# Optimization experiments

Hardware: AMD Instinct MI355X
Metric: run time of the kernel (lower is better)

## Reference

```python
import jax, jax.numpy as jnp
import numpy as np

N = 40000
E = 200000
D = 32
NUM_BANDS = 3
ORDER = 4
EPS = 1e-8
LN_EPS = 1e-5


def setup_inputs() -> dict:
    key = jax.random.key(0)
    ks = jax.random.split(key, 20)
    h = jax.random.normal(ks[0], (N, D), dtype=jnp.float32)
    Q = jax.random.normal(ks[1], (E, D, D), dtype=jnp.float32) / jnp.sqrt(jnp.float32(D))
    edge_index = jax.random.randint(ks[2], (2, E), 0, N, dtype=jnp.int32)
    coeffs = jnp.ones((NUM_BANDS, ORDER + 1), dtype=jnp.float32) / (ORDER + 1)
    s = 1.0 / np.sqrt(D)
    proj_W = jax.random.uniform(ks[3], (NUM_BANDS, D, D), minval=-s, maxval=s, dtype=jnp.float32)
    proj_b = jax.random.uniform(ks[4], (NUM_BANDS, D), minval=-s, maxval=s, dtype=jnp.float32)
    proj_g = jnp.ones((NUM_BANDS, D), dtype=jnp.float32)
    proj_beta = jnp.zeros((NUM_BANDS, D), dtype=jnp.float32)
    s3 = 1.0 / np.sqrt(NUM_BANDS * D)
    fus_W1 = jax.random.uniform(ks[5], (NUM_BANDS * D, D), minval=-s3, maxval=s3, dtype=jnp.float32)
    fus_b1 = jax.random.uniform(ks[6], (D,), minval=-s3, maxval=s3, dtype=jnp.float32)
    fus_g = jnp.ones((D,), dtype=jnp.float32)
    fus_beta = jnp.zeros((D,), dtype=jnp.float32)
    fus_W2 = jax.random.uniform(ks[7], (D, D), minval=-s, maxval=s, dtype=jnp.float32)
    fus_b2 = jax.random.uniform(ks[8], (D,), minval=-s, maxval=s, dtype=jnp.float32)
    return {"h": h, "Q": Q, "edge_index": edge_index, "coeffs": coeffs,
            "proj_W": proj_W, "proj_b": proj_b, "proj_g": proj_g, "proj_beta": proj_beta,
            "fus_W1": fus_W1, "fus_b1": fus_b1, "fus_g": fus_g, "fus_beta": fus_beta,
            "fus_W2": fus_W2, "fus_b2": fus_b2}


def _layer_norm(x, g, b):
    mu = x.mean(-1, keepdims=True)
    var = x.var(-1, keepdims=True)  # biased, as torch LayerNorm
    return (x - mu) / jnp.sqrt(var + LN_EPS) * g + b


def reference(h, Q, edge_index, coeffs, proj_W, proj_b, proj_g, proj_beta,
              fus_W1, fus_b1, fus_g, fus_beta, fus_W2, fus_b2):
    row, col = edge_index[0], edge_index[1]
    n = h.shape[0]
    ones_e = jnp.ones(row.shape[0], dtype=h.dtype)
    deg = (jax.ops.segment_sum(ones_e, row, num_segments=n)
           + jax.ops.segment_sum(ones_e, col, num_segments=n))  # [N]

    def matvec(x):
        # gather -> per-edge DxD bmm -> scatter_add; diag via degree
        Qh = jnp.einsum('eij,ej->ei', Q, x[col])          # [E, D]
        off = jax.ops.segment_sum(Qh, row, num_segments=n)  # [N, D]
        return deg[:, None] * x - off

    # power iteration for lambda_max (5 iters, fixed key for determinism)
    v = jax.random.normal(jax.random.key(42), h.shape, dtype=h.dtype)
    v = v / jnp.linalg.norm(v)
    lam = jnp.array(1.0, dtype=h.dtype)
    for _ in range(5):
        Lv = matvec(v)
        lam = (v * Lv).sum() / ((v * v).sum() + EPS)
        v = Lv / (jnp.linalg.norm(Lv) + EPS)
    lam = jnp.maximum(lam, 1.0)

    def L_tilde(x):
        return 2.0 / (lam + EPS) * matvec(x) - x

    bands = []
    for b_idx in range(NUM_BANDS):
        w = jax.nn.softmax(coeffs[b_idx])
        T_prev = h
        T_curr = L_tilde(h)
        res = w[0] * T_prev + w[1] * T_curr
        for k in range(2, ORDER + 1):
            T_next = 2.0 * L_tilde(T_curr) - T_prev
            res = res + w[k] * T_next
            T_prev, T_curr = T_curr, T_next
        p = jax.nn.silu(_layer_norm(res @ proj_W[b_idx] + proj_b[b_idx],
                                    proj_g[b_idx], proj_beta[b_idx]))
        bands.append(p)

    cat = jnp.concatenate(bands, axis=-1)  # [N, 3D]
    fused = jax.nn.silu(_layer_norm(cat @ fus_W1 + fus_b1, fus_g, fus_beta)) @ fus_W2 + fus_b2
    return h + fused
```

## Files before the change

kernel.cpp:

```cpp
#include <hip/hip_runtime.h>
#include <hip/hip_fp16.h>
#include <math.h>

#define NN 40000
#define EE 200000
#define DD 32
#define ND (NN * DD)
#define LNEPS 1e-5f

typedef float    fv4 __attribute__((ext_vector_type(4)));
typedef unsigned uv4 __attribute__((ext_vector_type(4)));

#define SLOT_S1    0
#define SLOT_S2    32
#define SLOT_ALPHA 48

__device__ __forceinline__ void threefry2x32(unsigned k0, unsigned k1,
                                             unsigned x0, unsigned x1,
                                             unsigned& o0, unsigned& o1) {
  const unsigned k2 = k0 ^ k1 ^ 0x1BD11BDAu;
  unsigned v0 = x0 + k0, v1 = x1 + k1;
#define TF_ROUND(r) { v0 += v1; v1 = (v1 << (r)) | (v1 >> (32 - (r))); v1 ^= v0; }
  TF_ROUND(13) TF_ROUND(15) TF_ROUND(26) TF_ROUND(6)
  v0 += k1; v1 += k2 + 1u;
  TF_ROUND(17) TF_ROUND(29) TF_ROUND(16) TF_ROUND(24)
  v0 += k2; v1 += k0 + 2u;
  TF_ROUND(13) TF_ROUND(15) TF_ROUND(26) TF_ROUND(6)
  v0 += k0; v1 += k1 + 3u;
  TF_ROUND(17) TF_ROUND(29) TF_ROUND(16) TF_ROUND(24)
  v0 += k1; v1 += k2 + 4u;
  TF_ROUND(13) TF_ROUND(15) TF_ROUND(26) TF_ROUND(6)
  v0 += k2; v1 += k0 + 5u;
#undef TF_ROUND
  o0 = v0; o1 = v1;
}

__device__ __forceinline__ float wave64_sum(float x) {
  for (int o = 32; o > 0; o >>= 1) x += __shfl_xor(x, o, 64);
  return x;
}
__device__ __forceinline__ float g32_sum(float x) {
  for (int o = 16; o > 0; o >>= 1) x += __shfl_xor(x, o, 32);
  return x;
}

__global__ void k_deg(const int* __restrict__ ei, float* __restrict__ deg,
                      int* __restrict__ hist) {
  int e = blockIdx.x * 256 + threadIdx.x;
  if (e < EE) {
    int r = ei[e];
    atomicAdd(deg + r, 1.0f);
    atomicAdd(deg + ei[EE + e], 1.0f);
    atomicAdd(hist + r, 1);
  }
}

__global__ __launch_bounds__(1024) void k_scan(const int* __restrict__ hist,
                                               int* __restrict__ row_start,
                                               int* __restrict__ cursor) {
  __shared__ int part[1024];
  const int t = threadIdx.x;
  const int base = t * 40;
  int s = 0;
  for (int i = base; i < base + 40 && i < NN; ++i) s += hist[i];
  part[t] = s;
  __syncthreads();
  for (int off = 1; off < 1024; off <<= 1) {
    int v = (t >= off) ? part[t - off] : 0;
    __syncthreads();
    part[t] += v;
    __syncthreads();
  }
  int ex = (t == 0) ? 0 : part[t - 1];
  for (int i = base; i < base + 40 && i < NN; ++i) {
    row_start[i] = ex;
    cursor[i] = ex;
    ex += hist[i];
  }
  if (t == 0) row_start[NN] = EE;
}

__global__ void k_genv(float* __restrict__ v) {
  int i = blockIdx.x * 256 + threadIdx.x;
  unsigned o0, o1;
  threefry2x32(0u, 42u, 0u, (unsigned)i, o0, o1);
  unsigned bits = o1;
  float f = __uint_as_float((bits >> 9) | 0x3f800000u) - 1.0f;
  const float lo = -0.99999994f;
  float u = fmaxf(lo, f * 2.0f + lo);
  v[i] = 1.41421354f * erfinvf(u);
}

__device__ __forceinline__ int clamp8(float q) {
  int v = (int)rintf(q);
  return v < -127 ? -127 : (v > 127 ? 127 : v);
}
__device__ __forceinline__ unsigned pack4v(fv4 q, float inv) {
  int q0 = clamp8(q.x * inv), q1 = clamp8(q.y * inv),
      q2 = clamp8(q.z * inv), q3 = clamp8(q.w * inv);
  return (q0 & 255) | ((q1 & 255) << 8) | ((q2 & 255) << 16) | ((q3 & 255) << 24);
}
__device__ __forceinline__ void dp4(unsigned u, fv4 xv, float& acc) {
  acc = fmaf((float)(signed char)(u),        xv.x, acc);
  acc = fmaf((float)(signed char)(u >> 8),   xv.y, acc);
  acc = fmaf((float)(signed char)(u >> 16),  xv.z, acc);
  acc = fmaf((float)(signed char)(u >> 24),  xv.w, acc);
}

__global__ __launch_bounds__(256) void k_cvt(const float* __restrict__ Q,
                                             const int* __restrict__ ei,
                                             int* __restrict__ cursor,
                                             char* __restrict__ Qi8,
                                             __half* __restrict__ Qs,
                                             int* __restrict__ cols) {
  const int slot = threadIdx.x >> 5;
  const int lane = threadIdx.x & 31;
  const int e = blockIdx.x * 8 + slot;
  const int row = ei[e];
  const int col = ei[EE + e];
  int pos = 0;
  if (lane == 0) pos = atomicAdd(cursor + row, 1);
  pos = __shfl(pos, 0, 32);
  const fv4* __restrict__ q4 =
      (const fv4*)(Q + (size_t)e * (DD * DD) + (size_t)lane * DD);
  fv4 qf[8];
#pragma unroll
  for (int k = 0; k < 8; ++k) qf[k] = __builtin_nontemporal_load(q4 + k);
  float m = 0.0f;
#pragma unroll
  for (int k = 0; k < 8; ++k) {
    m = fmaxf(m, fmaxf(fmaxf(fabsf(qf[k].x), fabsf(qf[k].y)),
                       fmaxf(fabsf(qf[k].z), fabsf(qf[k].w))));
  }
  __half sh = __float2half(m * (1.0f / 127.0f));
  float s = __half2float(sh);
  float inv = (s > 0.0f) ? 1.0f / s : 0.0f;
  uv4 pa, pb;
  pa.x = pack4v(qf[0], inv); pa.y = pack4v(qf[1], inv);
  pa.z = pack4v(qf[2], inv); pa.w = pack4v(qf[3], inv);
  pb.x = pack4v(qf[4], inv); pb.y = pack4v(qf[5], inv);
  pb.z = pack4v(qf[6], inv); pb.w = pack4v(qf[7], inv);
  uv4* __restrict__ qs = (uv4*)(Qi8 + (size_t)pos * (DD * DD) + (size_t)lane * DD);
  qs[0] = pa;
  qs[1] = pb;
  Qs[pos * DD + lane] = sh;
  if (lane == 0) cols[pos] = col;
}

__global__ __launch_bounds__(256) void k_gather(const float* __restrict__ x,
                                                const float* __restrict__ xprev,
                                                const char* __restrict__ Qi8,
                                                const __half* __restrict__ Qs,
                                                const int* __restrict__ cols,
                                                const int* __restrict__ row_start,
                                                const float* __restrict__ deg,
                                                const float* __restrict__ scal,
                                                float* __restrict__ out, int mode) {
  const int slot = threadIdx.x >> 5;
  const int lane = threadIdx.x & 31;
  const int r = blockIdx.x * 8 + slot;
  const int beg = row_start[r];
  const int end = row_start[r + 1];
  float off_acc = 0.0f;
  for (int p = beg; p < end; ++p) {
    const int col = cols[p];
    const fv4* __restrict__ x4 = (const fv4*)(x + (size_t)col * DD);
    fv4 xr[8];
#pragma unroll
    for (int k = 0; k < 8; ++k) xr[k] = x4[k];
    const uv4* __restrict__ q8 =
        (const uv4*)(Qi8 + (size_t)p * (DD * DD) + (size_t)lane * DD);
    uv4 pa = q8[0];
    uv4 pb = q8[1];
    float s = __half2float(Qs[p * DD + lane]);
    float d = 0.0f;
    dp4(pa.x, xr[0], d); dp4(pa.y, xr[1], d);
    dp4(pa.z, xr[2], d); dp4(pa.w, xr[3], d);
    dp4(pb.x, xr[4], d); dp4(pb.y, xr[5], d);
    dp4(pb.z, xr[6], d); dp4(pb.w, xr[7], d);
    off_acc = fmaf(s, d, off_acc);
  }
  const size_t idx = (size_t)r * DD + lane;
  const float xi = x[idx];
  const float dv = deg[r];
  float o;
  if (mode == 0)      o = dv * xi - off_acc;
  else if (mode == 1) o = scal[SLOT_ALPHA] * (dv * xi - off_acc) - xi;
  else                o = 2.0f * scal[SLOT_ALPHA] * (dv * xi - off_acc)
                          - 2.0f * xi - xprev[idx];
  out[idx] = o;
}

__global__ void k_pre(const float* __restrict__ x, const float* __restrict__ xprev,
                      const float* __restrict__ deg, const float* __restrict__ scal,
                      float* __restrict__ out, int mode) {
  int i = blockIdx.x * 256 + threadIdx.x;
  float d = deg[i >> 5];
  float xi = x[i];
  if (mode == 0)       out[i] = d * xi;
  else if (mode == 1)  out[i] = scal[SLOT_ALPHA] * d * xi - xi;
  else                 out[i] = 2.0f * scal[SLOT_ALPHA] * d * xi - 2.0f * xi - xprev[i];
}

__global__ __launch_bounds__(256) void k_matvec(const float* __restrict__ x,
                                                const float* __restrict__ Q,
                                                const int* __restrict__ ei,
                                                float* __restrict__ out,
                                                const float* __restrict__ scal,
                                                int use_alpha, float smul) {
  const int slot = threadIdx.x >> 5;
  const int lane = threadIdx.x & 31;
  const int e = blockIdx.x * 8 + slot;
  const float factor = use_alpha ? scal[SLOT_ALPHA] * smul : smul;
  const int row = ei[e];
  const int col = ei[EE + e];
  const fv4* __restrict__ x4 = (const fv4*)(x + (size_t)col * DD);
  fv4 xr[8];
#pragma unroll
  for (int k = 0; k < 8; ++k) xr[k] = x4[k];
  const fv4* __restrict__ q4 =
      (const fv4*)(Q + (size_t)e * (DD * DD) + (size_t)lane * DD);
  float acc = 0.0f;
#pragma unroll
  for (int k = 0; k < 8; ++k) {
    fv4 q = q4[k];
    acc = fmaf(q.x, xr[k].x, acc);
    acc = fmaf(q.y, xr[k].y, acc);
    acc = fmaf(q.z, xr[k].z, acc);
    acc = fmaf(q.w, xr[k].w, acc);
  }
  atomicAdd(out + (size_t)row * DD + lane, -factor * acc);
}

#define DOT_BLOCKS 640
__global__ void k_dots(const float* __restrict__ u4, const float* __restrict__ u5,
                       float* __restrict__ scal) {
  float s1 = 0.0f, s2 = 0.0f;
  for (int i = blockIdx.x * 256 + threadIdx.x; i < ND; i += DOT_BLOCKS * 256) {
    float a = u4[i], b = u5[i];
    s1 = fmaf(a, b, s1);
    s2 = fmaf(a, a, s2);
  }
  s1 = wave64_sum(s1);
  s2 = wave64_sum(s2);
  __shared__ float ls1[4], ls2[4];
  int w = threadIdx.x >> 6;
  if ((threadIdx.x & 63) == 0) { ls1[w] = s1; ls2[w] = s2; }
  __syncthreads();
  if (threadIdx.x == 0) {
    atomicAdd(scal + SLOT_S1, ls1[0] + ls1[1] + ls1[2] + ls1[3]);
    atomicAdd(scal + SLOT_S2, ls2[0] + ls2[1] + ls2[2] + ls2[3]);
  }
}

__global__ void k_alpha(float* __restrict__ scal) {
  float lam = scal[SLOT_S1] / scal[SLOT_S2] / (1.0f + 1e-8f);
  lam = fmaxf(lam, 1.0f);
  scal[SLOT_ALPHA] = 2.0f / (lam + 1e-8f);
}

__global__ __launch_bounds__(256) void k_fuse(
    const float* __restrict__ h,
    const float* __restrict__ T1, const float* __restrict__ T2,
    const float* __restrict__ T3, const float* __restrict__ T4,
    const float* __restrict__ coeffs,
    const float* __restrict__ projW, const float* __restrict__ projb,
    const float* __restrict__ projg, const float* __restrict__ projbeta,
    const float* __restrict__ fusW1, const float* __restrict__ fusb1,
    const float* __restrict__ fusg, const float* __restrict__ fusbeta,
    const float* __restrict__ fusW2, const float* __restrict__ fusb2,
    float* __restrict__ out) {
  __shared__ float s_res[8][3][DD];
  __shared__ float s_p[8][3 * DD];
  __shared__ float s_s[8][DD];
  const int slot = threadIdx.x >> 5;
  const int lane = threadIdx.x & 31;
  const int n = blockIdx.x * 8 + slot;

  float w[3][5];
#pragma unroll
  for (int b = 0; b < 3; ++b) {
    float m = -1e30f;
#pragma unroll
    for (int k = 0; k < 5; ++k) m = fmaxf(m, coeffs[b * 5 + k]);
    float s = 0.0f;
#pragma unroll
    for (int k = 0; k < 5; ++k) { w[b][k] = expf(coeffs[b * 5 + k] - m); s += w[b][k]; }
#pragma unroll
    for (int k = 0; k < 5; ++k) w[b][k] /= s;
  }

  const int idx = n * DD + lane;
  float hd = h[idx], t1 = T1[idx], t2 = T2[idx], t3 = T3[idx], t4 = T4[idx];
#pragma unroll
  for (int b = 0; b < 3; ++b)
    s_res[slot][b][lane] =
        w[b][0] * hd + w[b][1] * t1 + w[b][2] * t2 + w[b][3] * t3 + w[b][4] * t4;
  __syncthreads();

#pragma unroll
  for (int b = 0; b < 3; ++b) {
    float y = projb[b * DD + lane];
#pragma unroll
    for (int j = 0; j < DD; ++j)
      y = fmaf(s_res[slot][b][j], projW[(b * DD + j) * DD + lane], y);
    float mu = g32_sum(y) * (1.0f / DD);
    float d = y - mu;
    float var = g32_sum(d * d) * (1.0f / DD);
    float z = d * rsqrtf(var + LNEPS) * projg[b * DD + lane] + projbeta[b * DD + lane];
    float pb = z / (1.0f + expf(-z));
    s_p[slot][b * DD + lane] = pb;
  }
  __syncthreads();

  float y = fusb1[lane];
#pragma unroll
  for (int j = 0; j < 3 * DD; ++j)
    y = fmaf(s_p[slot][j], fusW1[j * DD + lane], y);
  float mu = g32_sum(y) * (1.0f / DD);
  float d = y - mu;
  float var = g32_sum(d * d) * (1.0f / DD);
  float z = d * rsqrtf(var + LNEPS) * fusg[lane] + fusbeta[lane];
  float sv = z / (1.0f + expf(-z));
  s_s[slot][lane] = sv;
  __syncthreads();

  float o = fusb2[lane];
#pragma unroll
  for (int j = 0; j < DD; ++j)
    o = fmaf(s_s[slot][j], fusW2[j * DD + lane], o);
  out[idx] = hd + o;
}

extern "C" void kernel_launch(void* const* d_in, const int* in_sizes, int n_in,
                              void* d_out, int out_size, void* d_ws, size_t ws_size,
                              hipStream_t stream) {
  (void)in_sizes; (void)n_in; (void)out_size;
  const float* h        = (const float*)d_in[0];
  const float* Q        = (const float*)d_in[1];
  const int*   ei       = (const int*)d_in[2];
  const float* coeffs   = (const float*)d_in[3];
  const float* projW    = (const float*)d_in[4];
  const float* projb    = (const float*)d_in[5];
  const float* projg    = (const float*)d_in[6];
  const float* projbeta = (const float*)d_in[7];
  const float* fusW1    = (const float*)d_in[8];
  const float* fusb1    = (const float*)d_in[9];
  const float* fusg     = (const float*)d_in[10];
  const float* fusbeta  = (const float*)d_in[11];
  const float* fusW2    = (const float*)d_in[12];
  const float* fusb2    = (const float*)d_in[13];
  float* out = (float*)d_out;

  const size_t qi_bytes  = (size_t)EE * DD * DD;
  const size_t qs_bytes  = (size_t)EE * DD * sizeof(__half);
  const size_t col_bytes = (size_t)EE * sizeof(int);
  const size_t idx_bytes = (size_t)(3 * NN + 2) * sizeof(int);
  const size_t f32_elems = 6u * (size_t)ND + NN + 64;
  const size_t need = qi_bytes + qs_bytes + col_bytes + idx_bytes +
                      f32_elems * sizeof(float) + 256;
  const bool fast = ws_size >= need;

  char*   Qi8 = (char*)d_ws;
  __half* Qs  = (__half*)((char*)d_ws + qi_bytes);
  int*  cols      = (int*)((char*)d_ws + qi_bytes + qs_bytes);
  int*  row_start = cols + EE;
  int*  cursor    = row_start + NN + 1;
  float* base = fast
      ? (float*)((char*)d_ws + ((qi_bytes + qs_bytes + col_bytes + idx_bytes + 255) & ~(size_t)255))
      : (float*)d_ws;
  float* uA   = base;
  float* uB   = uA + ND;
  float* T1   = uB + ND;
  float* T2   = T1 + ND;
  float* T3   = T2 + ND;
  float* T4   = T3 + ND;
  float* deg  = T4 + ND;
  float* scal = deg + NN;
  int*   hist = (int*)(scal + 64);

  (void)hipMemsetAsync(deg, 0, (2 * NN + 64) * sizeof(float), stream);

  k_deg<<<(EE + 255) / 256, 256, 0, stream>>>(ei, deg, hist);
  k_genv<<<ND / 256, 256, 0, stream>>>(uA);

  if (fast) {
    k_scan<<<1, 1024, 0, stream>>>(hist, row_start, cursor);
    k_cvt<<<EE / 8, 256, 0, stream>>>(Q, ei, cursor, Qi8, Qs, cols);

    float* cur = uA;
    float* nxt = uB;
    for (int it = 0; it < 5; ++it) {
      k_gather<<<NN / 8, 256, 0, stream>>>(cur, nullptr, Qi8, Qs, cols,
                                           row_start, deg, scal, nxt, 0);
      float* t = cur; cur = nxt; nxt = t;
    }
    k_dots<<<DOT_BLOCKS, 256, 0, stream>>>(nxt, cur, scal);
    k_alpha<<<1, 1, 0, stream>>>(scal);

    const float* xin[4]   = {h, T1, T2, T3};
    const float* prevs[4] = {nullptr, h, T1, T2};
    float* touts[4]       = {T1, T2, T3, T4};
    for (int k = 0; k < 4; ++k) {
      k_gather<<<NN / 8, 256, 0, stream>>>(xin[k], prevs[k], Qi8, Qs, cols,
                                           row_start, deg, scal, touts[k],
                                           k == 0 ? 1 : 2);
    }
  } else {
    float* cur = uA;
    float* nxt = uB;
    for (int it = 0; it < 5; ++it) {
      k_pre<<<ND / 256, 256, 0, stream>>>(cur, nullptr, deg, scal, nxt, 0);
      k_matvec<<<EE / 8, 256, 0, stream>>>(cur, Q, ei, nxt, scal, 0, 1.0f);
      float* t = cur; cur = nxt; nxt = t;
    }
    k_dots<<<DOT_BLOCKS, 256, 0, stream>>>(nxt, cur, scal);
    k_alpha<<<1, 1, 0, stream>>>(scal);
    const float* xin[4]   = {h, T1, T2, T3};
    const float* prevs[4] = {nullptr, h, T1, T2};
    float* touts[4]       = {T1, T2, T3, T4};
    for (int k = 0; k < 4; ++k) {
      k_pre<<<ND / 256, 256, 0, stream>>>(xin[k], prevs[k], deg, scal, touts[k],
                                          k == 0 ? 1 : 2);
      k_matvec<<<EE / 8, 256, 0, stream>>>(xin[k], Q, ei, touts[k], scal, 1,
                                           k == 0 ? 1.0f : 2.0f);
    }
  }

  k_fuse<<<NN / 8, 256, 0, stream>>>(h, T1, T2, T3, T4, coeffs,
                                     projW, projb, projg, projbeta,
                                     fusW1, fusb1, fusg, fusbeta,
                                     fusW2, fusb2, out);
}
```

Before: 1.037 ms.

## Process two edges per wave in gather SpMV with shuffled column indices

The gather kernel now assigns one full 64-lane wavefront per row instead of a 32-lane half, with each half of the wave handling alternate edges, and combines the two partial sums with a cross-half shuffle. Column indices are loaded cooperatively in chunks of 64 and broadcast by shuffle rather than read by every lane. The goal is more memory-level parallelism per row and fewer redundant index loads. The cost is twice as many launched blocks, and on odd-degree rows half the wave sits idle for the last edge.

```diff
diff --git a/kernel.cpp b/kernel.cpp
--- a/kernel.cpp
+++ b/kernel.cpp
@@ -156,39 +156,56 @@
                                                 const float* __restrict__ deg,
                                                 const float* __restrict__ scal,
                                                 float* __restrict__ out, int mode) {
-  const int slot = threadIdx.x >> 5;
-  const int lane = threadIdx.x & 31;
-  const int r = blockIdx.x * 8 + slot;
+  const int wid  = threadIdx.x >> 6;
+  const int lane = threadIdx.x & 63;
+  const int half = lane >> 5;
+  const int d    = lane & 31;
+  const int r = blockIdx.x * 4 + wid;
   const int beg = row_start[r];
   const int end = row_start[r + 1];
-  float off_acc = 0.0f;
-  for (int p = beg; p < end; ++p) {
-    const int col = cols[p];
-    const fv4* __restrict__ x4 = (const fv4*)(x + (size_t)col * DD);
-    fv4 xr[8];
-#pragma unroll
-    for (int k = 0; k < 8; ++k) xr[k] = x4[k];
-    const uv4* __restrict__ q8 =
-        (const uv4*)(Qi8 + (size_t)p * (DD * DD) + (size_t)lane * DD);
-    uv4 pa = q8[0];
-    uv4 pb = q8[1];
-    float s = __half2float(Qs[p * DD + lane]);
-    float d = 0.0f;
-    dp4(pa.x, xr[0], d); dp4(pa.y, xr[1], d);
-    dp4(pa.z, xr[2], d); dp4(pa.w, xr[3], d);
-    dp4(pb.x, xr[4], d); dp4(pb.y, xr[5], d);
-    dp4(pb.z, xr[6], d); dp4(pb.w, xr[7], d);
-    off_acc = fmaf(s, d, off_acc);
-  }
-  const size_t idx = (size_t)r * DD + lane;
-  const float xi = x[idx];
-  const float dv = deg[r];
-  float o;
-  if (mode == 0)      o = dv * xi - off_acc;
-  else if (mode == 1) o = scal[SLOT_ALPHA] * (dv * xi - off_acc) - xi;
-  else                o = 2.0f * scal[SLOT_ALPHA] * (dv * xi - off_acc)
-                          - 2.0f * xi - xprev[idx];
-  out[idx] = o;
+  const int degree = end - beg;
+
+  float acc = 0.0f;
+  for (int chunk = 0; chunk < degree; chunk += 64) {
+    const int nchunk = min(64, degree - chunk);
+    int myc = (lane < nchunk) ? cols[beg + chunk + lane] : 0;
+    for (int p0 = 0; p0 < nchunk; p0 += 2) {
+      const int p = p0 + half;
+      const bool act = p < nchunk;
+      const int col = __shfl(myc, p, 64);
+      const int pos = beg + chunk + p;
+      if (act) {
+        const fv4* __restrict__ x4 = (const fv4*)(x + (size_t)col * DD);
+        fv4 xr[8];
+#pragma unroll
+        for (int k = 0; k < 8; ++k) xr[k] = x4[k];
+        const uv4* __restrict__ q8 =
+            (const uv4*)(Qi8 + (size_t)pos * (DD * DD) + (size_t)d * DD);
+        uv4 pa = q8[0];
+        uv4 pb = q8[1];
+        float s = __half2float(Qs[pos * DD + d]);
+        float dot = 0.0f;
+        dp4(pa.x, xr[0], dot); dp4(pa.y, xr[1], dot);
+        dp4(pa.z, xr[2], dot); dp4(pa.w, xr[3], dot);
+        dp4(pb.x, xr[4], dot); dp4(pb.y, xr[5], dot);
+        dp4(pb.z, xr[6], dot); dp4(pb.w, xr[7], dot);
+        acc = fmaf(s, dot, acc);
+      }
+    }
+  }
+  acc += __shfl_xor(acc, 32, 64);
+
+  if (half == 0) {
+    const size_t idx = (size_t)r * DD + d;
+    const float xi = x[idx];
+    const float dv = deg[r];
+    float o;
+    if (mode == 0)      o = dv * xi - acc;
+    else if (mode == 1) o = scal[SLOT_ALPHA] * (dv * xi - acc) - xi;
+    else                o = 2.0f * scal[SLOT_ALPHA] * (dv * xi - acc)
+                            - 2.0f * xi - xprev[idx];
+    out[idx] = o;
+  }
 }
 
 __global__ void k_pre(const float* __restrict__ x, const float* __restrict__ xprev,
@@ -391,7 +408,7 @@
     float* cur = uA;
     float* nxt = uB;
     for (int it = 0; it < 5; ++it) {
-      k_gather<<<NN / 8, 256, 0, stream>>>(cur, nullptr, Qi8, Qs, cols,
+      k_gather<<<NN / 4, 256, 0, stream>>>(cur, nullptr, Qi8, Qs, cols,
                                            row_start, deg, scal, nxt, 0);
       float* t = cur; cur = nxt; nxt = t;
     }
@@ -402,7 +419,7 @@
     const float* prevs[4] = {nullptr, h, T1, T2};
     float* touts[4]       = {T1, T2, T3, T4};
     for (int k = 0; k < 4; ++k) {
-      k_gather<<<NN / 8, 256, 0, stream>>>(xin[k], prevs[k], Qi8, Qs, cols,
+      k_gather<<<NN / 4, 256, 0, stream>>>(xin[k], prevs[k], Qi8, Qs, cols,
                                            row_start, deg, scal, touts[k],
                                            k == 0 ? 1 : 2);
     }
```

Result: faster. 983.9 us (-5.1%).
